# Kernel tuning notes

Hardware: AMD Instinct MI355X
Metric: run time of the kernel (lower is better)

## Reference

```python
import jax, jax.numpy as jnp
import numpy as np

VOCAB = 100000
EDIM = 300
MUS = np.array([-0.9, -0.7, -0.5, -0.3, -0.1, 0.1, 0.3, 0.5, 0.7, 0.9, 1.0], dtype=np.float32)
SIGMAS = np.array([0.1] * 10 + [0.001], dtype=np.float32)


def setup_inputs() -> dict:
    key = jax.random.key(0)
    k1, k2, k3, k4, k5, k6 = jax.random.split(key, 6)
    B, Q, D = 128, 16, 1024
    doctoks = jax.random.randint(k1, (B, D), 0, VOCAB)
    querytoks = jax.random.randint(k2, (B, Q), 0, VOCAB)
    query_idf = jax.random.uniform(k3, (B, Q), dtype=jnp.float32)
    emb_table = jax.random.normal(k4, (VOCAB, EDIM), dtype=jnp.float32) * 0.1
    # pad token 0 -> zero embedding (padding_idx semantics)
    emb_table = emb_table.at[0].set(0.0)
    mus = jnp.asarray(MUS)
    sigmas = jnp.asarray(SIGMAS)
    K = mus.shape[0]
    fc_w = jax.random.normal(k5, (1, K), dtype=jnp.float32) * (1.0 / np.sqrt(K))
    fc_b = jax.random.normal(k6, (1,), dtype=jnp.float32) * 0.01
    return {"doctoks": doctoks, "querytoks": querytoks, "query_idf": query_idf,
            "emb_table": emb_table, "mus": mus, "sigmas": sigmas,
            "fc_w": fc_w, "fc_b": fc_b}


def reference(doctoks, querytoks, query_idf, emb_table, mus, sigmas, fc_w, fc_b):
    eps = 1e-9
    q_emb = emb_table[querytoks]                # [B,Q,E]
    d_emb = emb_table[doctoks]                  # [B,D,E]
    qn = q_emb / (jnp.linalg.norm(q_emb, axis=-1, keepdims=True) + eps)
    dn = d_emb / (jnp.linalg.norm(d_emb, axis=-1, keepdims=True) + eps)
    simmat = jnp.einsum('bqe,bde->bqd', qn, dn)  # cosine sim [B,Q,D]
    # zero out padded positions (token id 0)
    pad_mask = (querytoks != 0)[:, :, None] & (doctoks != 0)[:, None, :]
    simmat = jnp.where(pad_mask, simmat, 0.0)
    # RBF kernel bank broadcast at dim=1: [B,K,Q,D]
    diff = simmat[:, None, :, :] - mus[None, :, None, None]
    kernels = jnp.exp(-0.5 * diff * diff / (sigmas[None, :, None, None] ** 2))
    result = kernels.sum(axis=3)                 # [B,K,Q]
    mask = (simmat.sum(axis=2) != 0.0)[:, None, :]  # [B,1,Q] -> broadcasts over K
    mask = jnp.broadcast_to(mask, result.shape)
    result = jnp.where(mask, jnp.log(result + 1e-6), 0.0)
    result = result.sum(axis=2)                  # [B,K]
    scores = result @ fc_w.T + fc_b              # [B,1]
    return scores
```

## Files before the change

### kernel.cpp

```cpp
#include <hip/hip_runtime.h>

#define EDIM 300
#define NB   128
#define NQ   16
#define ND   1024
#define NK   11
#define BLOCK 256
#define TDOCS 256
#define BLOCKS_PER_B 4
#define DTILE 32
#define NTILE 8
#define NF4   75


__device__ __forceinline__ void gload16(const float* g, float* l) {
    __builtin_amdgcn_global_load_lds(
        (const __attribute__((address_space(1))) void*)g,
        (__attribute__((address_space(3))) void*)l, 16, 0, 0);
}

__global__ __launch_bounds__(BLOCK, 1) void knrm_main(
    const int*   __restrict__ dtoks,
    const int*   __restrict__ qtoks,
    const float* __restrict__ emb,
    const float* __restrict__ mus,
    const float* __restrict__ sigmas,
    float*       __restrict__ part) {
    __shared__ __align__(16) float qn_s[NQ * EDIM];
    __shared__ __align__(16) float dpan[2][DTILE * EDIM];
    __shared__ int   dtok_s[TDOCS];
    __shared__ float rs_s[NQ];

    const int blk   = blockIdx.x;
    const int b     = blk >> 2;
    const int dbase = (blk & 3) * TDOCS;
    const int tid   = threadIdx.x;
    const int lane  = tid & 63;
    const int w     = tid >> 6;

    dtok_s[tid] = dtoks[b * ND + dbase + tid];
#pragma unroll
    for (int i = 0; i < 5; ++i) {
        if (i < 4 || lane < 44) {
            int fi = w * 300 + i * 64 + lane;
            int q = fi / NF4, e4 = fi - q * NF4;
            gload16(emb + (size_t)qtoks[b * NQ + q] * EDIM + e4 * 4, qn_s + fi * 4);
        }
    }

#define STAGE(tb, dst) do {                                                    \
    _Pragma("unroll")                                                          \
    for (int i_ = 0; i_ < 10; ++i_) {                                          \
        if (i_ < 9 || lane < 24) {                                             \
            int fi_ = w * 600 + i_ * 64 + lane;                                \
            int r_ = fi_ / NF4, e4_ = fi_ - r_ * NF4;                          \
            gload16(emb + (size_t)dtok_s[(tb) * DTILE + r_] * EDIM + e4_ * 4,  \
                    (dst) + fi_ * 4);                                          \
        }                                                                      \
    } } while (0)

    STAGE(0, dpan[0]);

    __syncthreads();
    {
        int q = tid >> 4, j = tid & 15;
        float ss = 0.f;
        for (int e = j; e < EDIM; e += 16) { float v = qn_s[q * EDIM + e]; ss += v * v; }
        ss += __shfl_xor(ss, 1, 64);
        ss += __shfl_xor(ss, 2, 64);
        ss += __shfl_xor(ss, 4, 64);
        ss += __shfl_xor(ss, 8, 64);
        if (j == 0) rs_s[q] = 1.0f / (sqrtf(ss) + 1e-9f);
    }
    __syncthreads();
    for (int i = tid; i < NQ * NF4; i += BLOCK) {
        float4 v = ((float4*)qn_s)[i];
        float r = rs_s[i / NF4];
        v.x *= r; v.y *= r; v.z *= r; v.w *= r;
        ((float4*)qn_s)[i] = v;
    }

    const int d    = lane & 15;
    const int g    = lane >> 4;
    const int e4lo = g * 19;

    float mu[3], c2[3];
#pragma unroll
    for (int j = 0; j < 3; ++j) {
        int kk = g * 3 + j; if (kk > NK - 1) kk = NK - 1;
        mu[j] = mus[kk];
        float sg = sigmas[kk];
        c2[j] = -0.5f / (sg * sg);
    }
    float racc[12];
#pragma unroll
    for (int t = 0; t < 12; ++t) racc[t] = 0.f;

    for (int tb = 0; tb < NTILE; ++tb) {
        __syncthreads();
        if (tb + 1 < NTILE)
            STAGE(tb + 1, dpan[(tb + 1) & 1]);

        const float* cur = dpan[tb & 1];
        float sv[2][4], ssq[2];
#pragma unroll
        for (int m = 0; m < 2; ++m) { ssq[m] = 0.f;
#pragma unroll
            for (int qq = 0; qq < 4; ++qq) sv[m][qq] = 0.f; }

        const float* dr0 = cur + d * EDIM;
        const float* dr1 = cur + (d + 16) * EDIM;
        const float* qb  = qn_s + (w * 4) * EDIM;
#pragma unroll
        for (int i = 0; i < 19; ++i) {
            int e4 = e4lo + i;
            if (e4 < NF4) {
                float4 a = *(const float4*)(dr0 + e4 * 4);
                float4 c = *(const float4*)(dr1 + e4 * 4);
                ssq[0] += a.x*a.x + a.y*a.y + a.z*a.z + a.w*a.w;
                ssq[1] += c.x*c.x + c.y*c.y + c.z*c.z + c.w*c.w;
#pragma unroll
                for (int qq = 0; qq < 4; ++qq) {
                    float4 qv = *(const float4*)(qb + qq * EDIM + e4 * 4);
                    sv[0][qq] += qv.x*a.x + qv.y*a.y + qv.z*a.z + qv.w*a.w;
                    sv[1][qq] += qv.x*c.x + qv.y*c.y + qv.z*c.z + qv.w*c.w;
                }
            }
        }
#pragma unroll
        for (int m = 0; m < 2; ++m) {
            ssq[m] += __shfl_xor(ssq[m], 16, 64);
            ssq[m] += __shfl_xor(ssq[m], 32, 64);
#pragma unroll
            for (int qq = 0; qq < 4; ++qq) {
                sv[m][qq] += __shfl_xor(sv[m][qq], 16, 64);
                sv[m][qq] += __shfl_xor(sv[m][qq], 32, 64);
            }
        }
        float rn0 = 1.0f / (sqrtf(ssq[0]) + 1e-9f);
        float rn1 = 1.0f / (sqrtf(ssq[1]) + 1e-9f);
#pragma unroll
        for (int qq = 0; qq < 4; ++qq) {
            float s0 = sv[0][qq] * rn0;
            float s1 = sv[1][qq] * rn1;
#pragma unroll
            for (int j = 0; j < 3; ++j) {
                float e0 = s0 - mu[j], e1 = s1 - mu[j];
                racc[j * 4 + qq] += __expf(c2[j] * e0 * e0) + __expf(c2[j] * e1 * e1);
            }
        }
    }

#pragma unroll
    for (int t = 0; t < 12; ++t) {
        racc[t] += __shfl_xor(racc[t], 1, 64);
        racc[t] += __shfl_xor(racc[t], 2, 64);
        racc[t] += __shfl_xor(racc[t], 4, 64);
        racc[t] += __shfl_xor(racc[t], 8, 64);
    }
    if ((lane & 15) == 0) {
        const int kb = g * 3;
#pragma unroll
        for (int j = 0; j < 3; ++j) {
            if (g < 3 || j < 2) {
#pragma unroll
                for (int qq = 0; qq < 4; ++qq)
                    part[blk * (NK * NQ) + (kb + j) * NQ + (w * 4 + qq)] = racc[j * 4 + qq];
            }
        }
    }
}

__global__ void knrm_final(const float* __restrict__ part,
                           const int*   __restrict__ qtoks,
                           const float* __restrict__ fc_w,
                           const float* __restrict__ fc_b,
                           float*       __restrict__ out) {
    __shared__ float red[NK * NQ];
    __shared__ float ks[NK];
    int b = blockIdx.x;
    int t = threadIdx.x;
    if (t < NK * NQ) {
        int q = t & 15;
        float r = 0.f;
        for (int j = 0; j < BLOCKS_PER_B; ++j)
            r += part[(b * BLOCKS_PER_B + j) * (NK * NQ) + t];
        red[t] = (qtoks[b * NQ + q] != 0) ? logf(r + 1e-6f) : 0.f;
    }
    __syncthreads();
    if (t < NK) {
        float s = 0.f;
        for (int q = 0; q < NQ; ++q) s += red[t * NQ + q];
        ks[t] = s * fc_w[t];
    }
    __syncthreads();
    if (t == 0) {
        float s = fc_b[0];
        for (int k = 0; k < NK; ++k) s += ks[k];
        out[b] = s;
    }
}

extern "C" void kernel_launch(void* const* d_in, const int* in_sizes, int n_in,
                              void* d_out, int out_size, void* d_ws, size_t ws_size,
                              hipStream_t stream) {
    const int*   doctoks   = (const int*)  d_in[0];
    const int*   querytoks = (const int*)  d_in[1];
    const float* emb       = (const float*)d_in[3];
    const float* mus       = (const float*)d_in[4];
    const float* sigmas    = (const float*)d_in[5];
    const float* fc_w      = (const float*)d_in[6];
    const float* fc_b      = (const float*)d_in[7];
    float* out = (float*)d_out;

    float* part = (float*)d_ws;

    knrm_main<<<NB * BLOCKS_PER_B, BLOCK, 0, stream>>>(doctoks, querytoks, emb,
                                                       mus, sigmas, part);
    knrm_final<<<NB, 192, 0, stream>>>(part, querytoks, fc_w, fc_b, out);
}
```

Before: 245.9 us.

## Split query normalization into its own kernel and shrink doc tiles for occupancy

Query embedding normalization moves to a separate pre-kernel that writes normalized queries to workspace, and the main kernel loads them directly. The main kernel now uses 8 blocks per batch with 8-doc tiles and 16 tiles, and a new lane mapping gives each thread one doc and two kernel-bank slots, so fewer registers are needed and launch bounds allow 4 blocks per CU. The aim is to raise occupancy and parallelism on a grid that was only 512 blocks. The cost is an extra launch, a global round trip for the normalized queries, and more per-block overhead for reloading queries and shuffle reductions.

```diff
diff --git a/kernel.cpp b/kernel.cpp
--- a/kernel.cpp
+++ b/kernel.cpp
@@ -6,10 +6,10 @@
 #define ND   1024
 #define NK   11
 #define BLOCK 256
-#define TDOCS 256
-#define BLOCKS_PER_B 4
-#define DTILE 32
-#define NTILE 8
+#define TDOCS 128
+#define BLOCKS_PER_B 8
+#define DTILE 8
+#define NTILE 16
 #define NF4   75
 
 
@@ -19,48 +19,20 @@
         (__attribute__((address_space(3))) void*)l, 16, 0, 0);
 }
 
-__global__ __launch_bounds__(BLOCK, 1) void knrm_main(
-    const int*   __restrict__ dtoks,
-    const int*   __restrict__ qtoks,
-    const float* __restrict__ emb,
-    const float* __restrict__ mus,
-    const float* __restrict__ sigmas,
-    float*       __restrict__ part) {
+__global__ __launch_bounds__(BLOCK) void knrm_qnorm(
+    const int* __restrict__ qtoks, const float* __restrict__ emb,
+    float* __restrict__ qn_ws) {
     __shared__ __align__(16) float qn_s[NQ * EDIM];
-    __shared__ __align__(16) float dpan[2][DTILE * EDIM];
-    __shared__ int   dtok_s[TDOCS];
     __shared__ float rs_s[NQ];
-
-    const int blk   = blockIdx.x;
-    const int b     = blk >> 2;
-    const int dbase = (blk & 3) * TDOCS;
-    const int tid   = threadIdx.x;
-    const int lane  = tid & 63;
-    const int w     = tid >> 6;
-
-    dtok_s[tid] = dtoks[b * ND + dbase + tid];
+    const int b = blockIdx.x, tid = threadIdx.x, lane = tid & 63, w = tid >> 6;
 #pragma unroll
     for (int i = 0; i < 5; ++i) {
+        int fi = w * 300 + i * 64 + lane;
         if (i < 4 || lane < 44) {
-            int fi = w * 300 + i * 64 + lane;
             int q = fi / NF4, e4 = fi - q * NF4;
             gload16(emb + (size_t)qtoks[b * NQ + q] * EDIM + e4 * 4, qn_s + fi * 4);
         }
     }
-
-#define STAGE(tb, dst) do {                                                    \
-    _Pragma("unroll")                                                          \
-    for (int i_ = 0; i_ < 10; ++i_) {                                          \
-        if (i_ < 9 || lane < 24) {                                             \
-            int fi_ = w * 600 + i_ * 64 + lane;                                \
-            int r_ = fi_ / NF4, e4_ = fi_ - r_ * NF4;                          \
-            gload16(emb + (size_t)dtok_s[(tb) * DTILE + r_] * EDIM + e4_ * 4,  \
-                    (dst) + fi_ * 4);                                          \
-        }                                                                      \
-    } } while (0)
-
-    STAGE(0, dpan[0]);
-
     __syncthreads();
     {
         int q = tid >> 4, j = tid & 15;
@@ -73,100 +45,124 @@
         if (j == 0) rs_s[q] = 1.0f / (sqrtf(ss) + 1e-9f);
     }
     __syncthreads();
+    float4* dst = (float4*)(qn_ws + (size_t)b * NQ * EDIM);
     for (int i = tid; i < NQ * NF4; i += BLOCK) {
         float4 v = ((float4*)qn_s)[i];
         float r = rs_s[i / NF4];
         v.x *= r; v.y *= r; v.z *= r; v.w *= r;
-        ((float4*)qn_s)[i] = v;
-    }
-
-    const int d    = lane & 15;
-    const int g    = lane >> 4;
-    const int e4lo = g * 19;
-
-    float mu[3], c2[3];
+        dst[i] = v;
+    }
+}
+
+__global__ __launch_bounds__(BLOCK, 4) void knrm_main(
+    const int*   __restrict__ dtoks,
+    const float* __restrict__ qn_ws,
+    const float* __restrict__ emb,
+    const float* __restrict__ mus,
+    const float* __restrict__ sigmas,
+    float*       __restrict__ part) {
+    __shared__ __align__(16) float qn_s[NQ * EDIM];
+    __shared__ __align__(16) float dpan[2][DTILE * EDIM];
+    __shared__ int dtok_s[TDOCS];
+
+    const int blk   = blockIdx.x;
+    const int b     = blk >> 3;
+    const int dbase = (blk & 7) * TDOCS;
+    const int tid   = threadIdx.x;
+    const int lane  = tid & 63;
+    const int w     = tid >> 6;
+
+    if (tid < TDOCS) dtok_s[tid] = dtoks[b * ND + dbase + tid];
+    const float* qsrc = qn_ws + (size_t)b * NQ * EDIM;
 #pragma unroll
-    for (int j = 0; j < 3; ++j) {
-        int kk = g * 3 + j; if (kk > NK - 1) kk = NK - 1;
-        mu[j] = mus[kk];
-        float sg = sigmas[kk];
-        c2[j] = -0.5f / (sg * sg);
-    }
-    float racc[12];
-#pragma unroll
-    for (int t = 0; t < 12; ++t) racc[t] = 0.f;
+    for (int i = 0; i < 5; ++i) {
+        int fi = w * 300 + i * 64 + lane;
+        if (i < 4 || lane < 44) gload16(qsrc + fi * 4, qn_s + fi * 4);
+    }
+    __syncthreads();
+
+#define STAGE(tb, dst) do {                                                    \
+    _Pragma("unroll")                                                          \
+    for (int i_ = 0; i_ < 3; ++i_) {                                           \
+        if (i_ < 2 || lane < 22) {                                             \
+            int fi_ = w * 150 + i_ * 64 + lane;                                \
+            int r_ = fi_ / NF4, e4_ = fi_ - r_ * NF4;                          \
+            gload16(emb + (size_t)dtok_s[(tb) * DTILE + r_] * EDIM + e4_ * 4,  \
+                    (dst) + fi_ * 4);                                          \
+        }                                                                      \
+    } } while (0)
+
+    STAGE(0, dpan[0]);
+
+    const int d = lane & 7;
+    const int g = lane >> 3;
+    const float mua = mus[g];
+    const float sga = sigmas[g];
+    const float c2a = -0.5f / (sga * sga);
+    const int   kb  = (8 + g > NK - 1) ? NK - 1 : 8 + g;
+    const float mub = mus[kb];
+    const float sgb = sigmas[kb];
+    const float c2b = -0.5f / (sgb * sgb);
+
+    float ra0 = 0.f, ra1 = 0.f, ra2 = 0.f, ra3 = 0.f;
+    float rb0 = 0.f, rb1 = 0.f, rb2 = 0.f, rb3 = 0.f;
 
     for (int tb = 0; tb < NTILE; ++tb) {
         __syncthreads();
         if (tb + 1 < NTILE)
             STAGE(tb + 1, dpan[(tb + 1) & 1]);
 
-        const float* cur = dpan[tb & 1];
-        float sv[2][4], ssq[2];
+        const float* dr = dpan[tb & 1] + d * EDIM;
+        const float* qb = qn_s + (w * 4) * EDIM;
+        float sv0 = 0.f, sv1 = 0.f, sv2 = 0.f, sv3 = 0.f, ss = 0.f;
 #pragma unroll
-        for (int m = 0; m < 2; ++m) { ssq[m] = 0.f;
-#pragma unroll
-            for (int qq = 0; qq < 4; ++qq) sv[m][qq] = 0.f; }
-
-        const float* dr0 = cur + d * EDIM;
-        const float* dr1 = cur + (d + 16) * EDIM;
-        const float* qb  = qn_s + (w * 4) * EDIM;
-#pragma unroll
-        for (int i = 0; i < 19; ++i) {
-            int e4 = e4lo + i;
+        for (int i = 0; i < 10; ++i) {
+            int e4 = g * 10 + i;
             if (e4 < NF4) {
-                float4 a = *(const float4*)(dr0 + e4 * 4);
-                float4 c = *(const float4*)(dr1 + e4 * 4);
-                ssq[0] += a.x*a.x + a.y*a.y + a.z*a.z + a.w*a.w;
-                ssq[1] += c.x*c.x + c.y*c.y + c.z*c.z + c.w*c.w;
-#pragma unroll
-                for (int qq = 0; qq < 4; ++qq) {
-                    float4 qv = *(const float4*)(qb + qq * EDIM + e4 * 4);
-                    sv[0][qq] += qv.x*a.x + qv.y*a.y + qv.z*a.z + qv.w*a.w;
-                    sv[1][qq] += qv.x*c.x + qv.y*c.y + qv.z*c.z + qv.w*c.w;
-                }
+                float4 a  = *(const float4*)(dr + e4 * 4);
+                ss += a.x*a.x + a.y*a.y + a.z*a.z + a.w*a.w;
+                float4 q0 = *(const float4*)(qb + 0 * EDIM + e4 * 4);
+                float4 q1 = *(const float4*)(qb + 1 * EDIM + e4 * 4);
+                float4 q2 = *(const float4*)(qb + 2 * EDIM + e4 * 4);
+                float4 q3 = *(const float4*)(qb + 3 * EDIM + e4 * 4);
+                sv0 += q0.x*a.x + q0.y*a.y + q0.z*a.z + q0.w*a.w;
+                sv1 += q1.x*a.x + q1.y*a.y + q1.z*a.z + q1.w*a.w;
+                sv2 += q2.x*a.x + q2.y*a.y + q2.z*a.z + q2.w*a.w;
+                sv3 += q3.x*a.x + q3.y*a.y + q3.z*a.z + q3.w*a.w;
             }
         }
-#pragma unroll
-        for (int m = 0; m < 2; ++m) {
-            ssq[m] += __shfl_xor(ssq[m], 16, 64);
-            ssq[m] += __shfl_xor(ssq[m], 32, 64);
-#pragma unroll
-            for (int qq = 0; qq < 4; ++qq) {
-                sv[m][qq] += __shfl_xor(sv[m][qq], 16, 64);
-                sv[m][qq] += __shfl_xor(sv[m][qq], 32, 64);
-            }
-        }
-        float rn0 = 1.0f / (sqrtf(ssq[0]) + 1e-9f);
-        float rn1 = 1.0f / (sqrtf(ssq[1]) + 1e-9f);
-#pragma unroll
-        for (int qq = 0; qq < 4; ++qq) {
-            float s0 = sv[0][qq] * rn0;
-            float s1 = sv[1][qq] * rn1;
-#pragma unroll
-            for (int j = 0; j < 3; ++j) {
-                float e0 = s0 - mu[j], e1 = s1 - mu[j];
-                racc[j * 4 + qq] += __expf(c2[j] * e0 * e0) + __expf(c2[j] * e1 * e1);
-            }
-        }
-    }
-
-#pragma unroll
-    for (int t = 0; t < 12; ++t) {
-        racc[t] += __shfl_xor(racc[t], 1, 64);
-        racc[t] += __shfl_xor(racc[t], 2, 64);
-        racc[t] += __shfl_xor(racc[t], 4, 64);
-        racc[t] += __shfl_xor(racc[t], 8, 64);
-    }
-    if ((lane & 15) == 0) {
-        const int kb = g * 3;
-#pragma unroll
-        for (int j = 0; j < 3; ++j) {
-            if (g < 3 || j < 2) {
-#pragma unroll
-                for (int qq = 0; qq < 4; ++qq)
-                    part[blk * (NK * NQ) + (kb + j) * NQ + (w * 4 + qq)] = racc[j * 4 + qq];
-            }
+        ss  += __shfl_xor(ss, 8, 64);  ss  += __shfl_xor(ss, 16, 64);  ss  += __shfl_xor(ss, 32, 64);
+        sv0 += __shfl_xor(sv0, 8, 64); sv0 += __shfl_xor(sv0, 16, 64); sv0 += __shfl_xor(sv0, 32, 64);
+        sv1 += __shfl_xor(sv1, 8, 64); sv1 += __shfl_xor(sv1, 16, 64); sv1 += __shfl_xor(sv1, 32, 64);
+        sv2 += __shfl_xor(sv2, 8, 64); sv2 += __shfl_xor(sv2, 16, 64); sv2 += __shfl_xor(sv2, 32, 64);
+        sv3 += __shfl_xor(sv3, 8, 64); sv3 += __shfl_xor(sv3, 16, 64); sv3 += __shfl_xor(sv3, 32, 64);
+        const float rn = 1.0f / (sqrtf(ss) + 1e-9f);
+        const float s0 = sv0 * rn, s1 = sv1 * rn, s2 = sv2 * rn, s3 = sv3 * rn;
+        float e;
+        e = s0 - mua; ra0 += __expf(c2a * e * e);
+        e = s1 - mua; ra1 += __expf(c2a * e * e);
+        e = s2 - mua; ra2 += __expf(c2a * e * e);
+        e = s3 - mua; ra3 += __expf(c2a * e * e);
+        e = s0 - mub; rb0 += __expf(c2b * e * e);
+        e = s1 - mub; rb1 += __expf(c2b * e * e);
+        e = s2 - mub; rb2 += __expf(c2b * e * e);
+        e = s3 - mub; rb3 += __expf(c2b * e * e);
+    }
+
+#define RED(x) x += __shfl_xor(x, 1, 64); x += __shfl_xor(x, 2, 64); x += __shfl_xor(x, 4, 64)
+    RED(ra0); RED(ra1); RED(ra2); RED(ra3);
+    RED(rb0); RED(rb1); RED(rb2); RED(rb3);
+    if (d == 0) {
+        float* po = part + (size_t)blk * (NK * NQ);
+        po[g * NQ + (w * 4 + 0)] = ra0;
+        po[g * NQ + (w * 4 + 1)] = ra1;
+        po[g * NQ + (w * 4 + 2)] = ra2;
+        po[g * NQ + (w * 4 + 3)] = ra3;
+        if (g < 3) {
+            po[(8 + g) * NQ + (w * 4 + 0)] = rb0;
+            po[(8 + g) * NQ + (w * 4 + 1)] = rb1;
+            po[(8 + g) * NQ + (w * 4 + 2)] = rb2;
+            po[(8 + g) * NQ + (w * 4 + 3)] = rb3;
         }
     }
 }
@@ -184,7 +180,7 @@
         int q = t & 15;
         float r = 0.f;
         for (int j = 0; j < BLOCKS_PER_B; ++j)
-            r += part[(b * BLOCKS_PER_B + j) * (NK * NQ) + t];
+            r += part[(size_t)(b * BLOCKS_PER_B + j) * (NK * NQ) + t];
         red[t] = (qtoks[b * NQ + q] != 0) ? logf(r + 1e-6f) : 0.f;
     }
     __syncthreads();
@@ -213,9 +209,11 @@
     const float* fc_b      = (const float*)d_in[7];
     float* out = (float*)d_out;
 
-    float* part = (float*)d_ws;
-
-    knrm_main<<<NB * BLOCKS_PER_B, BLOCK, 0, stream>>>(doctoks, querytoks, emb,
+    float* part  = (float*)d_ws;
+    float* qn_ws = (float*)((char*)d_ws + (1 << 20));
+
+    knrm_qnorm<<<NB, BLOCK, 0, stream>>>(querytoks, emb, qn_ws);
+    knrm_main<<<NB * BLOCKS_PER_B, BLOCK, 0, stream>>>(doctoks, qn_ws, emb,
                                                        mus, sigmas, part);
     knrm_final<<<NB, 192, 0, stream>>>(part, querytoks, fc_w, fc_b, out);
 }
```

Result: faster. 233.4 us (-5.1%).
